# Performance work log

Hardware: AMD Instinct MI355X
Metric: run time of the kernel (lower is better)

## Reference

```python
import jax, jax.numpy as jnp
import numpy as np

S, B, H = 512, 32, 1024      # seq, batch, hidden_size
L = 4096                      # total spans (flattened ragged labels)
D = 1024                      # label_size (feature dim)
V = 32000                     # vocab size


def setup_inputs() -> dict:
    key = jax.random.key(0)
    ks = jax.random.split(key, 10)
    hidden = jax.random.normal(ks[0], (S, B, H), dtype=jnp.float32)
    span_bid = jax.random.randint(ks[1], (L,), 0, B)
    span_begin = jax.random.randint(ks[2], (L,), 0, S)
    span_end_m1 = jax.random.randint(ks[3], (L,), 0, S)  # (end - 1) index
    tags = jax.random.randint(ks[4], (L,), 0, V)
    # hidden2feature: Linear(2H -> D) with bias, Tanh
    W1 = jax.random.normal(ks[5], (D, 2 * H), dtype=jnp.float32) * (1.0 / np.sqrt(2 * H))
    b1 = jnp.zeros((D,), dtype=jnp.float32)
    # SoftmaxLoss h2o: Linear(D -> V, bias=False)
    Wout = jax.random.normal(ks[6], (V, D), dtype=jnp.float32) * (1.0 / np.sqrt(D))
    # discard probs from synthetic frequency counts
    counts = jax.random.uniform(ks[7], (V,), minval=1e-5, maxval=1.0)
    freqs = counts / counts.sum()
    discard_probs = jnp.clip(1.0 - jnp.sqrt(1e-4 / freqs), 0.0, None)
    return {"hidden": hidden, "W1": W1, "b1": b1, "Wout": Wout,
            "discard_probs": discard_probs, "span_bid": span_bid,
            "span_begin": span_begin, "span_end_m1": span_end_m1, "tags": tags}


def reference(hidden, W1, b1, Wout, discard_probs, span_bid, span_begin, span_end_m1, tags):
    # gather span endpoint embeddings: [L, H] each
    emb_b = hidden[span_begin, span_bid]
    emb_e = hidden[span_end_m1, span_bid]
    span_emb = jnp.concatenate([emb_b, emb_e], axis=-1)          # [L, 2H]
    feat = jnp.tanh(span_emb @ W1.T + b1)                        # [L, D]
    logits = feat @ Wout.T                                       # [L, V]
    logp = jax.nn.log_softmax(logits, axis=-1)
    nll = -jnp.take_along_axis(logp, tags[:, None], axis=-1)[:, 0]  # [L]
    scaled = 1.0 - discard_probs[tags]
    n_tags = tags.shape[0]
    return jnp.sum(nll * scaled) / (n_tags + 1e-5)
```

## Files before the change

kernel.cpp:

```cpp
#include <hip/hip_runtime.h>
#include <hip/hip_bf16.h>

#define LSPANS 4096
#define BB 32
#define HH 1024
#define DD 1024
#define VV 32000
#define K1 2048
#define NT2 250

typedef unsigned short u16;
typedef __attribute__((ext_vector_type(8))) short bf16x8v;
typedef __attribute__((ext_vector_type(4))) float f32x4v;

__device__ __forceinline__ u16 f2bf(float x) {
  union { float f; unsigned u; } v; v.f = x;
  unsigned r = (v.u >> 16) & 1u;
  return (u16)((v.u + 0x7fffu + r) >> 16);
}

__global__ void cvt_kernel(const float* __restrict__ in, u16* __restrict__ out, int n4) {
  int i = blockIdx.x * blockDim.x + threadIdx.x;
  int stride = gridDim.x * blockDim.x;
  for (; i < n4; i += stride) {
    float4 v = ((const float4*)in)[i];
    ushort4 o;
    o.x = f2bf(v.x); o.y = f2bf(v.y); o.z = f2bf(v.z); o.w = f2bf(v.w);
    ((ushort4*)out)[i] = o;
  }
}

__global__ void gather_kernel(const float* __restrict__ hidden,
                              const int* __restrict__ bid,
                              const int* __restrict__ sb,
                              const int* __restrict__ se,
                              u16* __restrict__ out) {
  int l = blockIdx.x;
  int t = threadIdx.x;
  int b  = bid[l];
  const float* p0 = hidden + ((size_t)sb[l] * BB + b) * HH;
  const float* p1 = hidden + ((size_t)se[l] * BB + b) * HH;
  u16* dst = out + (size_t)l * K1;
  float4 v0 = ((const float4*)p0)[t];
  float4 v1 = ((const float4*)p1)[t];
  ushort4 o0; o0.x = f2bf(v0.x); o0.y = f2bf(v0.y); o0.z = f2bf(v0.z); o0.w = f2bf(v0.w);
  ushort4 o1; o1.x = f2bf(v1.x); o1.y = f2bf(v1.y); o1.z = f2bf(v1.z); o1.w = f2bf(v1.w);
  ((ushort4*)dst)[t]          = o0;
  ((ushort4*)(dst + HH))[t]   = o1;
}

template <int K_, int EPI>
__launch_bounds__(256, 2)
__global__ void gemm_kernel(const u16* __restrict__ A, const u16* __restrict__ B,
                            int Ntot,
                            const float* __restrict__ bias, u16* __restrict__ feat_out,
                            const int* __restrict__ tags,
                            float* __restrict__ pmax, float* __restrict__ psum,
                            float* __restrict__ ltag) {
  __shared__ __align__(16) u16 As[128 * 64];
  __shared__ __align__(16) u16 Bs[128 * 64];
  __shared__ float rmax[2][128];
  __shared__ float rsum[2][128];
  __shared__ int   stags[128];

  const int tid  = threadIdx.x;
  const int lane = tid & 63;
  const int w    = tid >> 6;
  const int wm   = w & 1;
  const int wn   = w >> 1;
  const int q    = lane >> 4;
  const int lm   = lane & 15;
  const int mBase = blockIdx.x * 128;
  const int nBase = blockIdx.y * 128;

  if (EPI == 2 && tid < 128) stags[tid] = tags[mBase + tid];

  f32x4v acc[4][4];
#pragma unroll
  for (int i = 0; i < 4; ++i)
#pragma unroll
    for (int j = 0; j < 4; ++j) acc[i][j] = (f32x4v){0.f, 0.f, 0.f, 0.f};

  const int srow = w * 32 + (lane >> 3);
  const int scol = ((lane & 7) ^ (lane >> 3)) * 8;
  const u16* Ag = A + (size_t)(mBase + srow) * K_ + scol;
  const u16* Bg = B + (size_t)(nBase + srow) * K_ + scol;

  for (int k0 = 0; k0 < K_; k0 += 64) {
#pragma unroll
    for (int c = 0; c < 4; ++c) {
      __builtin_amdgcn_global_load_lds(
          (const __attribute__((address_space(1))) void*)(Ag + k0 + (size_t)c * 8 * K_),
          (__attribute__((address_space(3))) void*)(As + (w * 32 + c * 8) * 64), 16, 0, 0);
    }
#pragma unroll
    for (int c = 0; c < 4; ++c) {
      __builtin_amdgcn_global_load_lds(
          (const __attribute__((address_space(1))) void*)(Bg + k0 + (size_t)c * 8 * K_),
          (__attribute__((address_space(3))) void*)(Bs + (w * 32 + c * 8) * 64), 16, 0, 0);
    }
    __syncthreads();
#pragma unroll
    for (int kk = 0; kk < 64; kk += 32) {
      bf16x8v af[4], bfr[4];
      const int sw = lm & 7;
#pragma unroll
      for (int i = 0; i < 4; ++i) {
        int row = wm * 64 + i * 16 + lm;
        int kch = (kk >> 3) + q;
        af[i] = *(const bf16x8v*)(As + row * 64 + ((kch ^ sw) << 3));
      }
#pragma unroll
      for (int j = 0; j < 4; ++j) {
        int row = wn * 64 + j * 16 + lm;
        int kch = (kk >> 3) + q;
        bfr[j] = *(const bf16x8v*)(Bs + row * 64 + ((kch ^ sw) << 3));
      }
#pragma unroll
      for (int i = 0; i < 4; ++i)
#pragma unroll
        for (int j = 0; j < 4; ++j)
          acc[i][j] = __builtin_amdgcn_mfma_f32_16x16x32_bf16(af[i], bfr[j], acc[i][j], 0, 0, 0);
    }
    __syncthreads();
  }

  if constexpr (EPI == 1) {
    float bj[4];
#pragma unroll
    for (int j = 0; j < 4; ++j) bj[j] = bias[nBase + wn * 64 + j * 16 + lm];
#pragma unroll
    for (int i = 0; i < 4; ++i)
#pragma unroll
      for (int j = 0; j < 4; ++j)
#pragma unroll
        for (int r = 0; r < 4; ++r) {
          int tr = wm * 64 + i * 16 + q * 4 + r;
          int tc = wn * 64 + j * 16 + lm;
          float v = tanhf(acc[i][j][r] + bj[j]);
          feat_out[(size_t)(mBase + tr) * Ntot + nBase + tc] = f2bf(v);
        }
  }

  if constexpr (EPI == 2) {
#pragma unroll
    for (int i = 0; i < 4; ++i)
#pragma unroll
      for (int r = 0; r < 4; ++r) {
        float m = fmaxf(fmaxf(acc[i][0][r], acc[i][1][r]),
                        fmaxf(acc[i][2][r], acc[i][3][r]));
#pragma unroll
        for (int off = 1; off < 16; off <<= 1) m = fmaxf(m, __shfl_xor(m, off, 64));
        if (lm == 0) rmax[wn][wm * 64 + i * 16 + q * 4 + r] = m;
      }
    __syncthreads();
#pragma unroll
    for (int i = 0; i < 4; ++i)
#pragma unroll
      for (int r = 0; r < 4; ++r) {
        int tr = wm * 64 + i * 16 + q * 4 + r;
        float M = fmaxf(rmax[0][tr], rmax[1][tr]);
        float s = __expf(acc[i][0][r] - M) + __expf(acc[i][1][r] - M) +
                  __expf(acc[i][2][r] - M) + __expf(acc[i][3][r] - M);
#pragma unroll
        for (int off = 1; off < 16; off <<= 1) s += __shfl_xor(s, off, 64);
        if (lm == 0) rsum[wn][tr] = s;
      }
    __syncthreads();
    if (tid < 128) {
      float M = fmaxf(rmax[0][tid], rmax[1][tid]);
      float S = rsum[0][tid] + rsum[1][tid];
      pmax[(size_t)blockIdx.y * LSPANS + mBase + tid] = M;
      psum[(size_t)blockIdx.y * LSPANS + mBase + tid] = S;
    }
#pragma unroll
    for (int i = 0; i < 4; ++i)
#pragma unroll
      for (int r = 0; r < 4; ++r) {
        int tr = wm * 64 + i * 16 + q * 4 + r;
        int tg = stags[tr];
#pragma unroll
        for (int j = 0; j < 4; ++j) {
          int gc = nBase + wn * 64 + j * 16 + lm;
          if (tg == gc) ltag[mBase + tr] = acc[i][j][r];
        }
      }
  }
}

__global__ void finalize_kernel(const float* __restrict__ pmax, const float* __restrict__ psum,
                                const float* __restrict__ ltag, const int* __restrict__ tags,
                                const float* __restrict__ dprob, float* __restrict__ out) {
  int l = blockIdx.x * blockDim.x + threadIdx.x;
  const float* pm = pmax + l;
  const float* ps = psum + l;
  float M = -1e30f;
  for (int t = 0; t < NT2; ++t) M = fmaxf(M, pm[(size_t)t * LSPANS]);
  float S = 0.f;
  for (int t = 0; t < NT2; ++t) S += ps[(size_t)t * LSPANS] * __expf(pm[(size_t)t * LSPANS] - M);
  float nll = M + logf(S) - ltag[l];
  float wgt = 1.0f - dprob[tags[l]];
  float val = nll * wgt * (1.0f / (4096.0f + 1e-5f));
  __shared__ float red[4];
#pragma unroll
  for (int off = 32; off; off >>= 1) val += __shfl_down(val, off, 64);
  if ((threadIdx.x & 63) == 0) red[threadIdx.x >> 6] = val;
  __syncthreads();
  if (threadIdx.x == 0) atomicAdd(out, red[0] + red[1] + red[2] + red[3]);
}

extern "C" void kernel_launch(void* const* d_in, const int* in_sizes, int n_in,
                              void* d_out, int out_size, void* d_ws, size_t ws_size,
                              hipStream_t stream) {
  const float* hidden = (const float*)d_in[0];
  const float* W1     = (const float*)d_in[1];
  const float* b1     = (const float*)d_in[2];
  const float* Wout   = (const float*)d_in[3];
  const float* dprob  = (const float*)d_in[4];
  const int*   bid    = (const int*)d_in[5];
  const int*   sb     = (const int*)d_in[6];
  const int*   se     = (const int*)d_in[7];
  const int*   tags   = (const int*)d_in[8];
  float* out = (float*)d_out;

  char* ws = (char*)d_ws;
  u16* A1    = (u16*)ws;                 ws += (size_t)LSPANS * K1 * 2;
  u16* W1b   = (u16*)ws;                 ws += (size_t)DD * K1 * 2;
  u16* Woutb = (u16*)ws;                 ws += (size_t)VV * DD * 2;
  u16* feat  = (u16*)ws;                 ws += (size_t)LSPANS * DD * 2;
  float* pmax = (float*)ws;              ws += (size_t)NT2 * LSPANS * 4;
  float* psum = (float*)ws;              ws += (size_t)NT2 * LSPANS * 4;
  float* ltag = (float*)ws;              ws += (size_t)LSPANS * 4;

  hipMemsetAsync(d_out, 0, sizeof(float), stream);

  {
    int n4 = DD * K1 / 4;
    cvt_kernel<<<(n4 + 255) / 256, 256, 0, stream>>>(W1, W1b, n4);
  }
  {
    int n4 = VV * DD / 4;
    cvt_kernel<<<(n4 + 255) / 256, 256, 0, stream>>>(Wout, Woutb, n4);
  }
  gather_kernel<<<LSPANS, 256, 0, stream>>>(hidden, bid, sb, se, A1);

  gemm_kernel<K1, 1><<<dim3(LSPANS / 128, DD / 128), 256, 0, stream>>>(
      A1, W1b, DD, b1, feat, nullptr, nullptr, nullptr, nullptr);

  gemm_kernel<DD, 2><<<dim3(LSPANS / 128, NT2), 256, 0, stream>>>(
      feat, Woutb, VV, nullptr, nullptr, tags, pmax, psum, ltag);

  finalize_kernel<<<LSPANS / 256, 256, 0, stream>>>(pmax, psum, ltag, tags, dprob, out);
}
```

Baseline: 640.9 us.

## Use 256x256 double-buffered pipelined GEMM for the vocab projection with fused softmax

The big logits GEMM (4096x32000x1024) moves to a dedicated 512-thread kernel with 256x256 tiles, a two-stage LDS double buffer, explicit waitcnt and barrier scheduling, and MFMA priority raising, so global loads overlap compute. Larger tiles halve the number of partial softmax tiles (NT2 250 to 125), which reduces the partial max/sum traffic and the finalize loop. The first GEMM is specialized into a non-templated kernel. Costs are 128KB of LDS per block and more accumulator registers, which can limit occupancy. The hand-placed barriers also carry correctness risk if a wait is misplaced.

New measurement: 673.9 us. +5.2%, slower.

```diff
diff --git a/kernel.cpp b/kernel.cpp
--- a/kernel.cpp
+++ b/kernel.cpp
@@ -7,7 +7,7 @@
 #define DD 1024
 #define VV 32000
 #define K1 2048
-#define NT2 250
+#define NT2 125
 
 typedef unsigned short u16;
 typedef __attribute__((ext_vector_type(8))) short bf16x8v;
@@ -49,19 +49,12 @@
   ((ushort4*)(dst + HH))[t]   = o1;
 }
 
-template <int K_, int EPI>
 __launch_bounds__(256, 2)
-__global__ void gemm_kernel(const u16* __restrict__ A, const u16* __restrict__ B,
-                            int Ntot,
-                            const float* __restrict__ bias, u16* __restrict__ feat_out,
-                            const int* __restrict__ tags,
-                            float* __restrict__ pmax, float* __restrict__ psum,
-                            float* __restrict__ ltag) {
+__global__ void gemm128_kernel(const u16* __restrict__ A, const u16* __restrict__ B,
+                               int Ntot, const float* __restrict__ bias,
+                               u16* __restrict__ feat_out) {
   __shared__ __align__(16) u16 As[128 * 64];
   __shared__ __align__(16) u16 Bs[128 * 64];
-  __shared__ float rmax[2][128];
-  __shared__ float rsum[2][128];
-  __shared__ int   stags[128];
 
   const int tid  = threadIdx.x;
   const int lane = tid & 63;
@@ -73,8 +66,6 @@
   const int mBase = blockIdx.x * 128;
   const int nBase = blockIdx.y * 128;
 
-  if (EPI == 2 && tid < 128) stags[tid] = tags[mBase + tid];
-
   f32x4v acc[4][4];
 #pragma unroll
   for (int i = 0; i < 4; ++i)
@@ -83,20 +74,20 @@
 
   const int srow = w * 32 + (lane >> 3);
   const int scol = ((lane & 7) ^ (lane >> 3)) * 8;
-  const u16* Ag = A + (size_t)(mBase + srow) * K_ + scol;
-  const u16* Bg = B + (size_t)(nBase + srow) * K_ + scol;
-
-  for (int k0 = 0; k0 < K_; k0 += 64) {
+  const u16* Ag = A + (size_t)(mBase + srow) * K1 + scol;
+  const u16* Bg = B + (size_t)(nBase + srow) * K1 + scol;
+
+  for (int k0 = 0; k0 < K1; k0 += 64) {
 #pragma unroll
     for (int c = 0; c < 4; ++c) {
       __builtin_amdgcn_global_load_lds(
-          (const __attribute__((address_space(1))) void*)(Ag + k0 + (size_t)c * 8 * K_),
+          (const __attribute__((address_space(1))) void*)(Ag + k0 + (size_t)c * 8 * K1),
           (__attribute__((address_space(3))) void*)(As + (w * 32 + c * 8) * 64), 16, 0, 0);
     }
 #pragma unroll
     for (int c = 0; c < 4; ++c) {
       __builtin_amdgcn_global_load_lds(
-          (const __attribute__((address_space(1))) void*)(Bg + k0 + (size_t)c * 8 * K_),
+          (const __attribute__((address_space(1))) void*)(Bg + k0 + (size_t)c * 8 * K1),
           (__attribute__((address_space(3))) void*)(Bs + (w * 32 + c * 8) * 64), 16, 0, 0);
     }
     __syncthreads();
@@ -125,67 +116,198 @@
     __syncthreads();
   }
 
-  if constexpr (EPI == 1) {
-    float bj[4];
-#pragma unroll
-    for (int j = 0; j < 4; ++j) bj[j] = bias[nBase + wn * 64 + j * 16 + lm];
-#pragma unroll
-    for (int i = 0; i < 4; ++i)
-#pragma unroll
-      for (int j = 0; j < 4; ++j)
-#pragma unroll
-        for (int r = 0; r < 4; ++r) {
-          int tr = wm * 64 + i * 16 + q * 4 + r;
-          int tc = wn * 64 + j * 16 + lm;
-          float v = tanhf(acc[i][j][r] + bj[j]);
-          feat_out[(size_t)(mBase + tr) * Ntot + nBase + tc] = f2bf(v);
-        }
-  }
-
-  if constexpr (EPI == 2) {
-#pragma unroll
-    for (int i = 0; i < 4; ++i)
-#pragma unroll
-      for (int r = 0; r < 4; ++r) {
-        float m = fmaxf(fmaxf(acc[i][0][r], acc[i][1][r]),
-                        fmaxf(acc[i][2][r], acc[i][3][r]));
-#pragma unroll
-        for (int off = 1; off < 16; off <<= 1) m = fmaxf(m, __shfl_xor(m, off, 64));
-        if (lm == 0) rmax[wn][wm * 64 + i * 16 + q * 4 + r] = m;
-      }
-    __syncthreads();
-#pragma unroll
-    for (int i = 0; i < 4; ++i)
+  float bj[4];
+#pragma unroll
+  for (int j = 0; j < 4; ++j) bj[j] = bias[nBase + wn * 64 + j * 16 + lm];
+#pragma unroll
+  for (int i = 0; i < 4; ++i)
+#pragma unroll
+    for (int j = 0; j < 4; ++j)
 #pragma unroll
       for (int r = 0; r < 4; ++r) {
         int tr = wm * 64 + i * 16 + q * 4 + r;
-        float M = fmaxf(rmax[0][tr], rmax[1][tr]);
-        float s = __expf(acc[i][0][r] - M) + __expf(acc[i][1][r] - M) +
-                  __expf(acc[i][2][r] - M) + __expf(acc[i][3][r] - M);
-#pragma unroll
-        for (int off = 1; off < 16; off <<= 1) s += __shfl_xor(s, off, 64);
-        if (lm == 0) rsum[wn][tr] = s;
+        int tc = wn * 64 + j * 16 + lm;
+        float v = tanhf(acc[i][j][r] + bj[j]);
+        feat_out[(size_t)(mBase + tr) * Ntot + nBase + tc] = f2bf(v);
       }
-    __syncthreads();
-    if (tid < 128) {
-      float M = fmaxf(rmax[0][tid], rmax[1][tid]);
-      float S = rsum[0][tid] + rsum[1][tid];
-      pmax[(size_t)blockIdx.y * LSPANS + mBase + tid] = M;
-      psum[(size_t)blockIdx.y * LSPANS + mBase + tid] = S;
-    }
+}
+
+#define STAGE256(pp, k0) do {                                                       \
+  _Pragma("unroll")                                                                 \
+  for (int c = 0; c < 4; ++c)                                                       \
+    __builtin_amdgcn_global_load_lds(                                               \
+        (const __attribute__((address_space(1))) void*)(Ag + (k0) + (size_t)c * 8 * DD), \
+        (__attribute__((address_space(3))) void*)(&As[pp][(w * 32 + c * 8) * 64]), 16, 0, 0); \
+  _Pragma("unroll")                                                                 \
+  for (int c = 0; c < 4; ++c)                                                       \
+    __builtin_amdgcn_global_load_lds(                                               \
+        (const __attribute__((address_space(1))) void*)(Bg + (k0) + (size_t)c * 8 * DD), \
+        (__attribute__((address_space(3))) void*)(&Bs[pp][(w * 32 + c * 8) * 64]), 16, 0, 0); \
+} while (0)
+
+__launch_bounds__(512, 2)
+__global__ void gemm256_kernel(const u16* __restrict__ A, const u16* __restrict__ B,
+                               const int* __restrict__ tags,
+                               float* __restrict__ pmax, float* __restrict__ psum,
+                               float* __restrict__ ltag) {
+  __shared__ __align__(16) u16 As[2][256 * 64];
+  __shared__ __align__(16) u16 Bs[2][256 * 64];
+  __shared__ float rmax[4][256];
+  __shared__ float rsum[4][256];
+  __shared__ int   stags[256];
+
+  const int tid  = threadIdx.x;
+  const int lane = tid & 63;
+  const int w    = tid >> 6;
+  const int wm   = w >> 2;
+  const int wn   = w & 3;
+  const int q    = lane >> 4;
+  const int lm   = lane & 15;
+  const int sw   = lm & 7;
+  const int mBase = blockIdx.x * 256;
+  const int nBase = blockIdx.y * 256;
+
+  if (tid < 256) stags[tid] = tags[mBase + tid];
+
+  f32x4v acc[8][4];
+#pragma unroll
+  for (int i = 0; i < 8; ++i)
+#pragma unroll
+    for (int j = 0; j < 4; ++j) acc[i][j] = (f32x4v){0.f, 0.f, 0.f, 0.f};
+
+  const int srow = w * 32 + (lane >> 3);
+  const int scol = ((lane & 7) ^ (lane >> 3)) * 8;
+  const u16* Ag = A + (size_t)(mBase + srow) * DD + scol;
+  const u16* Bg = B + (size_t)(nBase + srow) * DD + scol;
+
+  const int aoff = (wm * 128 + lm) * 64;
+  const int boff = (wn * 64 + lm) * 64;
+  const int c0 = (q ^ sw) << 3;
+  const int c1 = ((q + 4) ^ sw) << 3;
+
+  STAGE256(0, 0);
+  STAGE256(1, 64);
+  asm volatile("s_waitcnt vmcnt(8)" ::: "memory");
+  __builtin_amdgcn_s_barrier();
+  __builtin_amdgcn_sched_barrier(0);
+
+  const int NT = DD / 64;
+#pragma unroll 2
+  for (int t = 0; t < NT; ++t) {
+    const int p = t & 1;
+    const u16* Asp = &As[p][0];
+    const u16* Bsp = &Bs[p][0];
+    bf16x8v a0[4], a1[4], b0[4], b1[4];
+
+#pragma unroll
+    for (int i = 0; i < 4; ++i) a0[i] = *(const bf16x8v*)(Asp + aoff + i * 1024 + c0);
+#pragma unroll
+    for (int j = 0; j < 4; ++j) b0[j] = *(const bf16x8v*)(Bsp + boff + j * 1024 + c0);
+    __builtin_amdgcn_s_barrier();
+    asm volatile("s_waitcnt lgkmcnt(0)" ::: "memory");
+    __builtin_amdgcn_sched_barrier(0);
+    __builtin_amdgcn_s_setprio(1);
 #pragma unroll
     for (int i = 0; i < 4; ++i)
 #pragma unroll
-      for (int r = 0; r < 4; ++r) {
-        int tr = wm * 64 + i * 16 + q * 4 + r;
-        int tg = stags[tr];
-#pragma unroll
-        for (int j = 0; j < 4; ++j) {
-          int gc = nBase + wn * 64 + j * 16 + lm;
-          if (tg == gc) ltag[mBase + tr] = acc[i][j][r];
-        }
+      for (int j = 0; j < 4; ++j)
+        acc[i][j] = __builtin_amdgcn_mfma_f32_16x16x32_bf16(a0[i], b0[j], acc[i][j], 0, 0, 0);
+    __builtin_amdgcn_s_setprio(0);
+    __builtin_amdgcn_s_barrier();
+
+#pragma unroll
+    for (int i = 0; i < 4; ++i) a1[i] = *(const bf16x8v*)(Asp + aoff + (i + 4) * 1024 + c0);
+#pragma unroll
+    for (int j = 0; j < 4; ++j) b1[j] = *(const bf16x8v*)(Bsp + boff + j * 1024 + c1);
+    __builtin_amdgcn_s_barrier();
+    asm volatile("s_waitcnt lgkmcnt(0)" ::: "memory");
+    __builtin_amdgcn_sched_barrier(0);
+    __builtin_amdgcn_s_setprio(1);
+#pragma unroll
+    for (int i = 0; i < 4; ++i)
+#pragma unroll
+      for (int j = 0; j < 4; ++j)
+        acc[4 + i][j] = __builtin_amdgcn_mfma_f32_16x16x32_bf16(a1[i], b0[j], acc[4 + i][j], 0, 0, 0);
+    __builtin_amdgcn_s_setprio(0);
+    __builtin_amdgcn_s_barrier();
+
+#pragma unroll
+    for (int i = 0; i < 4; ++i) a0[i] = *(const bf16x8v*)(Asp + aoff + i * 1024 + c1);
+#pragma unroll
+    for (int i = 0; i < 4; ++i) a1[i] = *(const bf16x8v*)(Asp + aoff + (i + 4) * 1024 + c1);
+    __builtin_amdgcn_s_barrier();
+    asm volatile("s_waitcnt lgkmcnt(0)" ::: "memory");
+    __builtin_amdgcn_sched_barrier(0);
+    __builtin_amdgcn_s_setprio(1);
+#pragma unroll
+    for (int i = 0; i < 4; ++i)
+#pragma unroll
+      for (int j = 0; j < 4; ++j)
+        acc[i][j] = __builtin_amdgcn_mfma_f32_16x16x32_bf16(a0[i], b1[j], acc[i][j], 0, 0, 0);
+    __builtin_amdgcn_s_setprio(0);
+    __builtin_amdgcn_s_barrier();
+
+    if (t + 2 < NT) STAGE256(p, (t + 2) * 64);
+    __builtin_amdgcn_s_barrier();
+    __builtin_amdgcn_s_setprio(1);
+#pragma unroll
+    for (int i = 0; i < 4; ++i)
+#pragma unroll
+      for (int j = 0; j < 4; ++j)
+        acc[4 + i][j] = __builtin_amdgcn_mfma_f32_16x16x32_bf16(a1[i], b1[j], acc[4 + i][j], 0, 0, 0);
+    __builtin_amdgcn_s_setprio(0);
+    if (t + 2 < NT) {
+      asm volatile("s_waitcnt vmcnt(8)" ::: "memory");
+    } else if (t + 1 < NT) {
+      asm volatile("s_waitcnt vmcnt(0)" ::: "memory");
+    }
+    __builtin_amdgcn_s_barrier();
+  }
+
+#pragma unroll
+  for (int i = 0; i < 8; ++i)
+#pragma unroll
+    for (int r = 0; r < 4; ++r) {
+      float m = fmaxf(fmaxf(acc[i][0][r], acc[i][1][r]),
+                      fmaxf(acc[i][2][r], acc[i][3][r]));
+#pragma unroll
+      for (int off = 1; off < 16; off <<= 1) m = fmaxf(m, __shfl_xor(m, off, 64));
+      if (lm == 0) rmax[wn][wm * 128 + i * 16 + q * 4 + r] = m;
+    }
+  __syncthreads();
+#pragma unroll
+  for (int i = 0; i < 8; ++i)
+#pragma unroll
+    for (int r = 0; r < 4; ++r) {
+      int tr = wm * 128 + i * 16 + q * 4 + r;
+      float M = fmaxf(fmaxf(rmax[0][tr], rmax[1][tr]),
+                      fmaxf(rmax[2][tr], rmax[3][tr]));
+      float s = __expf(acc[i][0][r] - M) + __expf(acc[i][1][r] - M) +
+                __expf(acc[i][2][r] - M) + __expf(acc[i][3][r] - M);
+#pragma unroll
+      for (int off = 1; off < 16; off <<= 1) s += __shfl_xor(s, off, 64);
+      if (lm == 0) rsum[wn][tr] = s;
+    }
+  __syncthreads();
+  if (tid < 256) {
+    float M = fmaxf(fmaxf(rmax[0][tid], rmax[1][tid]),
+                    fmaxf(rmax[2][tid], rmax[3][tid]));
+    float S = rsum[0][tid] + rsum[1][tid] + rsum[2][tid] + rsum[3][tid];
+    pmax[(size_t)blockIdx.y * LSPANS + mBase + tid] = M;
+    psum[(size_t)blockIdx.y * LSPANS + mBase + tid] = S;
+  }
+#pragma unroll
+  for (int i = 0; i < 8; ++i)
+#pragma unroll
+    for (int r = 0; r < 4; ++r) {
+      int tr = wm * 128 + i * 16 + q * 4 + r;
+      int tg = stags[tr];
+#pragma unroll
+      for (int j = 0; j < 4; ++j) {
+        int gc = nBase + wn * 64 + j * 16 + lm;
+        if (tg == gc) ltag[mBase + tr] = acc[i][j][r];
       }
-  }
+    }
 }
 
 __global__ void finalize_kernel(const float* __restrict__ pmax, const float* __restrict__ psum,
@@ -244,11 +366,11 @@
   }
   gather_kernel<<<LSPANS, 256, 0, stream>>>(hidden, bid, sb, se, A1);
 
-  gemm_kernel<K1, 1><<<dim3(LSPANS / 128, DD / 128), 256, 0, stream>>>(
-      A1, W1b, DD, b1, feat, nullptr, nullptr, nullptr, nullptr);
-
-  gemm_kernel<DD, 2><<<dim3(LSPANS / 128, NT2), 256, 0, stream>>>(
-      feat, Woutb, VV, nullptr, nullptr, tags, pmax, psum, ltag);
+  gemm128_kernel<<<dim3(LSPANS / 128, DD / 128), 256, 0, stream>>>(
+      A1, W1b, DD, b1, feat);
+
+  gemm256_kernel<<<dim3(LSPANS / 256, VV / 256), 512, 0, stream>>>(
+      feat, Woutb, tags, pmax, psum, ltag);
 
   finalize_kernel<<<LSPANS / 256, 256, 0, stream>>>(pmax, psum, ltag, tags, dprob, out);
 }
```
